# Kernel tuning notes

Measured on AMD Instinct MI355X. Metric: run time of the kernel, lower is better.

## Reference

```python
import jax, jax.numpy as jnp
import numpy as np

N = 100000      # graph nodes
M = 100000      # meta-graph nodes appended after graph nodes
F_IN = 128
HID = 64
NCLASS = 2
E = 1600000
L = 3           # n_layers
ALPHA = 0.2     # LeakyReLU negative slope (args.alpha)


def leaky(x):
    return jax.nn.leaky_relu(x, negative_slope=ALPHA)


def gcn_conv(x, src, dst, W, b, n):
    """PyG GCNConv: add self-loops, symmetric D^-1/2 (A+I) D^-1/2 X W + b."""
    loop = jnp.arange(n, dtype=src.dtype)
    s = jnp.concatenate([src, loop])
    d = jnp.concatenate([dst, loop])
    deg = jax.ops.segment_sum(jnp.ones(d.shape, x.dtype), d, num_segments=n)
    dinv = jnp.where(deg > 0, jax.lax.rsqrt(jnp.maximum(deg, 1.0)), 0.0)
    h = x @ W                                   # [n, out]
    msg = h[s] * (dinv[s] * dinv[d])[:, None]   # gather + edge-normalize
    return jax.ops.segment_sum(msg, d, num_segments=n) + b


def _uniform(k, shape, fan_in):
    s = 1.0 / np.sqrt(fan_in)
    return jax.random.uniform(k, shape, jnp.float32, -s, s)


def setup_inputs():
    key = jax.random.key(0)
    ks = jax.random.split(key, 14)
    x = jax.random.normal(ks[0], (N, F_IN), jnp.float32)
    meta_x = jax.random.normal(ks[1], (M, F_IN), jnp.float32)
    edge_index = jax.random.randint(ks[2], (2, E), 0, N, dtype=jnp.int32)
    # meta_edge_index: node i -> node2idx[i] + N, then add_self_loops over N+M nodes
    node2idx = jax.random.randint(ks[3], (N,), 0, M, dtype=jnp.int32)
    src = jnp.concatenate([jnp.arange(N, dtype=jnp.int32), jnp.arange(N + M, dtype=jnp.int32)])
    dst = jnp.concatenate([node2idx + N, jnp.arange(N + M, dtype=jnp.int32)])
    meta_edge_index = jnp.stack([src, dst])
    params = {
        "W_lin": _uniform(ks[4], (F_IN, HID), F_IN),
        "b_lin": jnp.zeros((HID,), jnp.float32),
        "W_meta_lin": _uniform(ks[5], (F_IN, HID), F_IN),
        "b_meta_lin": jnp.zeros((HID,), jnp.float32),
        "Ws": _uniform(ks[6], (L, HID, HID), HID),
        "bs": jnp.zeros((L, HID), jnp.float32),
        "W_mg": _uniform(ks[7], (HID, HID), HID),
        "b_mg": jnp.zeros((HID,), jnp.float32),
        "W_cls": _uniform(ks[8], (HID, NCLASS), HID),
        "b_cls": jnp.zeros((NCLASS,), jnp.float32),
    }
    return {"x": x, "meta_x": meta_x, "edge_index": edge_index,
            "meta_edge_index": meta_edge_index, **params}


def reference(x, meta_x, edge_index, meta_edge_index,
              W_lin, b_lin, W_meta_lin, b_meta_lin,
              Ws, bs, W_mg, b_mg, W_cls, b_cls):
    h = leaky(x @ W_lin + b_lin)                      # [N, HID]
    mh = leaky(meta_x @ W_meta_lin + b_meta_lin)      # [M, HID]
    src, dst = edge_index[0], edge_index[1]
    for i in range(L):  # dropout is identity in eval mode
        h = leaky(gcn_conv(h, src, dst, Ws[i], bs[i], N))
    z = jnp.concatenate([h, mh], axis=0)              # [N+M, HID]
    z = leaky(gcn_conv(z, meta_edge_index[0], meta_edge_index[1], W_mg, b_mg, N + M))
    logits = z @ W_cls + b_cls                        # [N+M, NCLASS]
    return jax.nn.log_softmax(logits, axis=1)
```

## Files before the change

kernel.cpp:

```cpp
#include <hip/hip_runtime.h>
#include <math.h>

#define ALPHA 0.2f

__device__ __forceinline__ float leaky(float x){ return x > 0.f ? x : ALPHA*x; }
__device__ __forceinline__ float bcast(float v, int l){
  return __int_as_float(__builtin_amdgcn_readlane(__float_as_int(v), l));
}
__device__ __forceinline__ int rdlane_i(int v, int l){
  return __builtin_amdgcn_readlane(v, l);
}

static inline int cdiv(long a, long b){ return (int)((a + b - 1)/b); }

__global__ void k_count_dual(const int* __restrict__ dstA, int nA, int* __restrict__ cntA,
                             const int* __restrict__ dstB, int nB, int* __restrict__ cntB){
  int i = blockIdx.x*blockDim.x + threadIdx.x;
  if(i < nA) atomicAdd(&cntA[dstA[i]], 1);
  else if(i < nA + nB) atomicAdd(&cntB[dstB[i - nA]], 1);
}

__global__ void k_dinv_dual(const int* __restrict__ cntA, float* __restrict__ dinvA, int nA,
                            const int* __restrict__ cntB, float* __restrict__ dinvB, int nB){
  int i = blockIdx.x*blockDim.x + threadIdx.x;
  if(i < nA) dinvA[i] = rsqrtf((float)(cntA[i]+1));
  else if(i < nA + nB){ int j = i - nA; dinvB[j] = rsqrtf((float)(cntB[j]+1)); }
}

__global__ void k_scan1_dual(const int* __restrict__ cntA, int* __restrict__ exA,
                             int* __restrict__ bsA, int nA, int nbA,
                             const int* __restrict__ cntB, int* __restrict__ exB,
                             int* __restrict__ bsB, int nB){
  const int* cnt; int* ex; int* bs; int n; int blk;
  if((int)blockIdx.x < nbA){ cnt=cntA; ex=exA; bs=bsA; n=nA; blk=blockIdx.x; }
  else                     { cnt=cntB; ex=exB; bs=bsB; n=nB; blk=blockIdx.x-nbA; }
  __shared__ int s[256];
  int i = blk*256 + threadIdx.x;
  int v = (i<n) ? cnt[i] : 0;
  s[threadIdx.x]=v; __syncthreads();
  #pragma unroll
  for(int off=1; off<256; off<<=1){
    int t = (threadIdx.x>=(unsigned)off) ? s[threadIdx.x-off] : 0;
    __syncthreads();
    s[threadIdx.x]+=t;
    __syncthreads();
  }
  if(i<n) ex[i] = s[threadIdx.x]-v;
  if(threadIdx.x==255) bs[blk]=s[255];
}

__global__ void k_scan2_dual(int* __restrict__ bsA, int nbA, int* __restrict__ bsB, int nbB){
  __shared__ int s[1024];
  {
    int v = ((int)threadIdx.x<nbA) ? bsA[threadIdx.x] : 0;
    s[threadIdx.x]=v; __syncthreads();
    #pragma unroll
    for(int off=1; off<1024; off<<=1){
      int t = (threadIdx.x>=(unsigned)off) ? s[threadIdx.x-off] : 0;
      __syncthreads();
      s[threadIdx.x]+=t;
      __syncthreads();
    }
    if((int)threadIdx.x<nbA) bsA[threadIdx.x] = s[threadIdx.x]-v;
    __syncthreads();
  }
  {
    int v = ((int)threadIdx.x<nbB) ? bsB[threadIdx.x] : 0;
    s[threadIdx.x]=v; __syncthreads();
    #pragma unroll
    for(int off=1; off<1024; off<<=1){
      int t = (threadIdx.x>=(unsigned)off) ? s[threadIdx.x-off] : 0;
      __syncthreads();
      s[threadIdx.x]+=t;
      __syncthreads();
    }
    if((int)threadIdx.x<nbB) bsB[threadIdx.x] = s[threadIdx.x]-v;
  }
}

__global__ void k_scan3_dual(int* __restrict__ exA, const int* __restrict__ bsA,
                             int nA, int nbA, int totA,
                             int* __restrict__ exB, const int* __restrict__ bsB,
                             int nB, int totB){
  int* ex; const int* bs; int n; int blk; int tot;
  if((int)blockIdx.x < nbA){ ex=exA; bs=bsA; n=nA; blk=blockIdx.x; tot=totA; }
  else                     { ex=exB; bs=bsB; n=nB; blk=blockIdx.x-nbA; tot=totB; }
  int i = blk*256 + threadIdx.x;
  if(i<n && blk>0) ex[i] += bs[blk];
  if(blk==0 && threadIdx.x==0) ex[n] = tot;
}

__global__ void k_fill_dual(const int* __restrict__ eiA, int nA,
                            const int* __restrict__ rpA, int* __restrict__ curA,
                            int* __restrict__ ceA,
                            const int* __restrict__ eiB, int nB,
                            const int* __restrict__ rpB, int* __restrict__ curB,
                            int* __restrict__ ceB){
  int i = blockIdx.x*blockDim.x + threadIdx.x;
  if(i < nA){
    int s = eiA[i], d = eiA[nA + i];
    int pos = rpA[d] + atomicAdd(&curA[d], 1);
    ceA[pos] = s;
  } else if(i < nA + nB){
    int j = i - nA;
    int s = eiB[j], d = eiB[nB + j];
    int pos = rpB[d] + atomicAdd(&curB[d], 1);
    ceB[pos] = s;
  }
}

template<int K, int LEAKY_IN, int EPI>
__global__ __launch_bounds__(256) void k_gemm(const float* __restrict__ X,
                                              const float* __restrict__ W,
                                              const float* __restrict__ b,
                                              float* __restrict__ out, int rows){
  int lane = threadIdx.x & 63;
  int gw = (blockIdx.x*256 + threadIdx.x) >> 6;
  int nw = (gridDim.x*256) >> 6;
  float wcol[K];
  #pragma unroll
  for(int k=0;k<K;k++) wcol[k] = W[(size_t)k*64 + lane];
  float bl = EPI ? b[lane] : 0.f;
  for(int row = gw; row < rows; row += nw){
    const float* xr = X + (size_t)row*K;
    float a0=0.f, a1=0.f, a2=0.f, a3=0.f;
    #pragma unroll
    for(int kk=0; kk<K; kk+=64){
      float xv = xr[kk + lane];
      if(LEAKY_IN) xv = leaky(xv);
      #pragma unroll
      for(int k=0;k<64;k+=4){
        a0 = fmaf(bcast(xv, k+0), wcol[kk+k+0], a0);
        a1 = fmaf(bcast(xv, k+1), wcol[kk+k+1], a1);
        a2 = fmaf(bcast(xv, k+2), wcol[kk+k+2], a2);
        a3 = fmaf(bcast(xv, k+3), wcol[kk+k+3], a3);
      }
    }
    float r = (a0+a1)+(a2+a3);
    if(EPI) r = leaky(r + bl);
    out[(size_t)row*64 + lane] = r;
  }
}

__device__ __forceinline__ float agg_acc(const float* __restrict__ h2,
                                         const int* __restrict__ rowptr,
                                         const int* __restrict__ ce,
                                         const float* __restrict__ dinv,
                                         const float* __restrict__ b,
                                         int i, int c){
  float dv = dinv[i];
  int start = rowptr[i], end = rowptr[i+1];
  float a0 = b[c] + h2[(size_t)i*64+c]*dv*dv, a1=0.f, a2=0.f, a3=0.f;
  int lane8 = c & 7;
  for(int j = start; j < end; j += 8){
    int idx = j + lane8; idx = (idx < end) ? idx : end-1;
    int sv = ce[idx];
    float dwv = dinv[sv];
    #pragma unroll
    for(int k=0;k<8;k+=4){
      int   s0 = rdlane_i(sv, k+0), s1 = rdlane_i(sv, k+1);
      int   s2 = rdlane_i(sv, k+2), s3 = rdlane_i(sv, k+3);
      float w0 = bcast(dwv, k+0), w1 = bcast(dwv, k+1);
      float w2 = bcast(dwv, k+2), w3 = bcast(dwv, k+3);
      float g0 = h2[(size_t)s0*64 + c];
      float g1 = h2[(size_t)s1*64 + c];
      float g2 = h2[(size_t)s2*64 + c];
      float g3 = h2[(size_t)s3*64 + c];
      w0 = (j+k+0 < end) ? w0*dv : 0.f;
      w1 = (j+k+1 < end) ? w1*dv : 0.f;
      w2 = (j+k+2 < end) ? w2*dv : 0.f;
      w3 = (j+k+3 < end) ? w3*dv : 0.f;
      a0 = fmaf(g0, w0, a0);
      a1 = fmaf(g1, w1, a1);
      a2 = fmaf(g2, w2, a2);
      a3 = fmaf(g3, w3, a3);
    }
  }
  return (a0+a1)+(a2+a3);
}

template<int LEAKY_OUT>
__global__ __launch_bounds__(256) void k_aggregate(const float* __restrict__ h2,
                            const int* __restrict__ rowptr,
                            const int* __restrict__ ce,
                            const float* __restrict__ dinv, const float* __restrict__ b,
                            float* __restrict__ out, int n){
  int tid = blockIdx.x*blockDim.x + threadIdx.x;
  int i = tid>>6, c = tid&63;
  if(i>=n) return;
  float acc = agg_acc(h2, rowptr, ce, dinv, b, i, c);
  out[(size_t)i*64+c] = LEAKY_OUT ? leaky(acc) : acc;
}

__global__ __launch_bounds__(256) void k_agg_cls(const float* __restrict__ h2,
                            const int* __restrict__ rowptr,
                            const int* __restrict__ ce,
                            const float* __restrict__ dinv, const float* __restrict__ b,
                            const float* __restrict__ Wc, const float* __restrict__ bc,
                            float* __restrict__ out, int n){
  int tid = blockIdx.x*blockDim.x + threadIdx.x;
  int i = tid>>6, c = tid&63;
  if(i>=n) return;
  float acc = agg_acc(h2, rowptr, ce, dinv, b, i, c);
  float zv = leaky(acc);
  float s0 = zv * Wc[c*2+0];
  float s1 = zv * Wc[c*2+1];
  #pragma unroll
  for(int off=32; off; off>>=1){
    s0 += __shfl_down(s0, off);
    s1 += __shfl_down(s1, off);
  }
  if(c==0){
    float l0 = s0 + bc[0], l1 = s1 + bc[1];
    float m  = fmaxf(l0,l1);
    float lse = m + logf(expf(l0-m)+expf(l1-m));
    out[(size_t)i*2+0] = l0 - lse;
    out[(size_t)i*2+1] = l1 - lse;
  }
}

extern "C" void kernel_launch(void* const* d_in, const int* in_sizes, int n_in,
                              void* d_out, int out_size, void* d_ws, size_t ws_size,
                              hipStream_t stream) {
  const float* x      = (const float*)d_in[0];
  const float* meta_x = (const float*)d_in[1];
  const int*   ei     = (const int*)d_in[2];
  const int*   mei    = (const int*)d_in[3];
  const float* W_lin  = (const float*)d_in[4];
  const float* b_lin  = (const float*)d_in[5];
  const float* W_meta = (const float*)d_in[6];
  const float* b_meta = (const float*)d_in[7];
  const float* Ws     = (const float*)d_in[8];
  const float* bs_    = (const float*)d_in[9];
  const float* W_mg   = (const float*)d_in[10];
  const float* b_mg   = (const float*)d_in[11];
  const float* W_cls  = (const float*)d_in[12];
  const float* b_cls  = (const float*)d_in[13];
  float* out = (float*)d_out;

  const int N  = in_sizes[0]/128;
  const int M  = in_sizes[1]/128;
  const int E  = in_sizes[2]/2;
  const int ME = in_sizes[3]/2;
  const int NM = N + M;

  char* ws = (char*)d_ws;
  size_t off = 0;
  auto alloc = [&](size_t bytes)->void*{ void* p = ws + off; off += (bytes + 255) & ~(size_t)255; return p; };
  float* zbuf  = (float*)alloc((size_t)NM*64*4);
  size_t hwords = (size_t)(2*N > NM ? 2*N : NM)*64;
  float* hreg  = (float*)alloc(hwords*4);
  float* hA = hreg, *hB = hreg + (size_t)N*64;
  float* z2 = hreg;
  int*  ce_g = (int*)alloc((size_t)E*4);
  int*  ce_m = (int*)alloc((size_t)ME*4);
  char* zero_base = ws + off;
  int* cnt_g    = (int*)alloc((size_t)N*4);
  int* cnt_m    = (int*)alloc((size_t)NM*4);
  int* cur_g    = (int*)alloc((size_t)N*4);
  int* cur_m    = (int*)alloc((size_t)NM*4);
  size_t zero_bytes = (ws + off) - zero_base;
  int* rowptr_g = (int*)alloc((size_t)(N+1)*4);
  int* rowptr_m = (int*)alloc((size_t)(NM+1)*4);
  int* bsumA    = (int*)alloc(1024*4);
  int* bsumB    = (int*)alloc(1024*4);
  float* dinv_g = (float*)alloc((size_t)N*4);
  float* dinv_m = (float*)alloc((size_t)NM*4);
  (void)ws_size; (void)n_in; (void)out_size;

  const int B = 256;
  const int nbA = cdiv(N, 256), nbB = cdiv(NM, 256);

  (void)hipMemsetAsync(zero_base, 0, zero_bytes, stream);

  k_count_dual<<<cdiv((long)E+ME,B), B, 0, stream>>>(ei+E, E, cnt_g, mei+ME, ME, cnt_m);
  k_dinv_dual<<<cdiv((long)N+NM,B), B, 0, stream>>>(cnt_g, dinv_g, N, cnt_m, dinv_m, NM);

  k_scan1_dual<<<nbA+nbB, 256, 0, stream>>>(cnt_g, rowptr_g, bsumA, N, nbA,
                                            cnt_m, rowptr_m, bsumB, NM);
  k_scan2_dual<<<1, 1024, 0, stream>>>(bsumA, nbA, bsumB, nbB);
  k_scan3_dual<<<nbA+nbB, 256, 0, stream>>>(rowptr_g, bsumA, N, nbA, E,
                                            rowptr_m, bsumB, NM, ME);
  k_fill_dual<<<cdiv((long)E+ME,B), B, 0, stream>>>(ei, E, rowptr_g, cur_g, ce_g,
                                                    mei, ME, rowptr_m, cur_m, ce_m);

  k_gemm<128,0,1><<<1024, 256, 0, stream>>>(x,      W_lin,  b_lin,  hA,                 N);
  k_gemm<128,0,1><<<1024, 256, 0, stream>>>(meta_x, W_meta, b_meta, zbuf + (size_t)N*64, M);

  float* cin = hA; float* tmp = hB;
  for(int l=0; l<3; ++l){
    const float* Wl = Ws + (size_t)l*64*64;
    const float* bl = bs_ + (size_t)l*64;
    if(l==0) k_gemm<64,0,0><<<2048, 256, 0, stream>>>(cin, Wl, nullptr, tmp, N);
    else     k_gemm<64,1,0><<<2048, 256, 0, stream>>>(cin, Wl, nullptr, tmp, N);
    if(l<2) k_aggregate<0><<<cdiv(N,4), B, 0, stream>>>(tmp, rowptr_g, ce_g, dinv_g, bl, cin, N);
    else    k_aggregate<1><<<cdiv(N,4), B, 0, stream>>>(tmp, rowptr_g, ce_g, dinv_g, bl, zbuf, N);
  }

  k_gemm<64,0,0><<<2048, 256, 0, stream>>>(zbuf, W_mg, nullptr, z2, NM);
  k_agg_cls<<<cdiv(NM,4), B, 0, stream>>>(z2, rowptr_m, ce_m, dinv_m, b_mg,
                                          W_cls, b_cls, out, NM);
}
```

Baseline: 758.7 us.

## Fuse aggregate-then-transform GCN layers and build CSR via two-level bucketing

Result: slower. 961.6 us (+26.7%).

```diff
diff --git a/kernel.cpp b/kernel.cpp
--- a/kernel.cpp
+++ b/kernel.cpp
@@ -79,55 +79,82 @@
 }
 
 __global__ void k_scan3_dual(int* __restrict__ exA, const int* __restrict__ bsA,
-                             int nA, int nbA, int totA,
+                             int nA, int nbA, int totA, int* __restrict__ bcurA,
                              int* __restrict__ exB, const int* __restrict__ bsB,
-                             int nB, int totB){
-  int* ex; const int* bs; int n; int blk; int tot;
-  if((int)blockIdx.x < nbA){ ex=exA; bs=bsA; n=nA; blk=blockIdx.x; tot=totA; }
-  else                     { ex=exB; bs=bsB; n=nB; blk=blockIdx.x-nbA; tot=totB; }
+                             int nB, int totB, int* __restrict__ bcurB){
+  int* ex; const int* bs; int n; int blk; int tot; int* bcur;
+  if((int)blockIdx.x < nbA){ ex=exA; bs=bsA; n=nA; blk=blockIdx.x; tot=totA; bcur=bcurA; }
+  else                     { ex=exB; bs=bsB; n=nB; blk=blockIdx.x-nbA; tot=totB; bcur=bcurB; }
   int i = blk*256 + threadIdx.x;
-  if(i<n && blk>0) ex[i] += bs[blk];
+  if(i<n){
+    int v = ex[i] + (blk>0 ? bs[blk] : 0);
+    ex[i] = v;
+    if((i&63)==0) bcur[i>>6] = v;
+  }
   if(blk==0 && threadIdx.x==0) ex[n] = tot;
 }
 
-__global__ void k_fill_dual(const int* __restrict__ eiA, int nA,
-                            const int* __restrict__ rpA, int* __restrict__ curA,
-                            int* __restrict__ ceA,
-                            const int* __restrict__ eiB, int nB,
-                            const int* __restrict__ rpB, int* __restrict__ curB,
-                            int* __restrict__ ceB){
+__global__ void k_bucket_dual(const int* __restrict__ eiA, int nA,
+                              int* __restrict__ bcurA, int2* __restrict__ tmpA,
+                              const int* __restrict__ eiB, int nB,
+                              int* __restrict__ bcurB, int2* __restrict__ tmpB){
   int i = blockIdx.x*blockDim.x + threadIdx.x;
   if(i < nA){
-    int s = eiA[i], d = eiA[nA + i];
-    int pos = rpA[d] + atomicAdd(&curA[d], 1);
-    ceA[pos] = s;
+    int s = eiA[i], d = eiA[nA+i];
+    int pos = atomicAdd(&bcurA[d>>6], 1);
+    tmpA[pos] = make_int2(s, d);
   } else if(i < nA + nB){
     int j = i - nA;
-    int s = eiB[j], d = eiB[nB + j];
-    int pos = rpB[d] + atomicAdd(&curB[d], 1);
-    ceB[pos] = s;
-  }
-}
-
-template<int K, int LEAKY_IN, int EPI>
-__global__ __launch_bounds__(256) void k_gemm(const float* __restrict__ X,
-                                              const float* __restrict__ W,
-                                              const float* __restrict__ b,
-                                              float* __restrict__ out, int rows){
+    int s = eiB[j], d = eiB[nB+j];
+    int pos = atomicAdd(&bcurB[d>>6], 1);
+    tmpB[pos] = make_int2(s, d);
+  }
+}
+
+__global__ __launch_bounds__(256) void k_place_dual(
+    const int2* __restrict__ tmpA, const int* __restrict__ rpA, int* __restrict__ ceA,
+    int nnA, int nbkA,
+    const int2* __restrict__ tmpB, const int* __restrict__ rpB, int* __restrict__ ceB,
+    int nnB){
+  const int2* tmp; const int* rp; int* ce; int nn; int b;
+  if((int)blockIdx.x < nbkA){ tmp=tmpA; rp=rpA; ce=ceA; nn=nnA; b=blockIdx.x; }
+  else                      { tmp=tmpB; rp=rpB; ce=ceB; nn=nnB; b=blockIdx.x-nbkA; }
+  __shared__ int lcur[64];
+  __shared__ int lrp[65];
+  int base = b<<6;
+  int t = threadIdx.x;
+  if(t<65){
+    int node = base + t; if(node > nn) node = nn;
+    lrp[t] = rp[node];
+    if(t<64) lcur[t] = 0;
+  }
+  __syncthreads();
+  int start = lrp[0], end = lrp[64];
+  for(int j = start + t; j < end; j += 256){
+    int2 r = tmp[j];
+    int dl = r.y - base;
+    int pos = lrp[dl] + atomicAdd(&lcur[dl], 1);
+    ce[pos] = r.x;
+  }
+}
+
+__global__ __launch_bounds__(256) void k_linear128(const float* __restrict__ X,
+                                                   const float* __restrict__ W,
+                                                   const float* __restrict__ b,
+                                                   float* __restrict__ out, int rows){
   int lane = threadIdx.x & 63;
   int gw = (blockIdx.x*256 + threadIdx.x) >> 6;
   int nw = (gridDim.x*256) >> 6;
-  float wcol[K];
+  float wcol[128];
   #pragma unroll
-  for(int k=0;k<K;k++) wcol[k] = W[(size_t)k*64 + lane];
-  float bl = EPI ? b[lane] : 0.f;
+  for(int k=0;k<128;k++) wcol[k] = W[(size_t)k*64 + lane];
+  float bl = b[lane];
   for(int row = gw; row < rows; row += nw){
-    const float* xr = X + (size_t)row*K;
+    const float* xr = X + (size_t)row*128;
     float a0=0.f, a1=0.f, a2=0.f, a3=0.f;
     #pragma unroll
-    for(int kk=0; kk<K; kk+=64){
+    for(int kk=0; kk<128; kk+=64){
       float xv = xr[kk + lane];
-      if(LEAKY_IN) xv = leaky(xv);
       #pragma unroll
       for(int k=0;k<64;k+=4){
         a0 = fmaf(bcast(xv, k+0), wcol[kk+k+0], a0);
@@ -136,86 +163,79 @@
         a3 = fmaf(bcast(xv, k+3), wcol[kk+k+3], a3);
       }
     }
-    float r = (a0+a1)+(a2+a3);
-    if(EPI) r = leaky(r + bl);
-    out[(size_t)row*64 + lane] = r;
-  }
-}
-
-__device__ __forceinline__ float agg_acc(const float* __restrict__ h2,
-                                         const int* __restrict__ rowptr,
-                                         const int* __restrict__ ce,
-                                         const float* __restrict__ dinv,
-                                         const float* __restrict__ b,
-                                         int i, int c){
-  float dv = dinv[i];
-  int start = rowptr[i], end = rowptr[i+1];
-  float a0 = b[c] + h2[(size_t)i*64+c]*dv*dv, a1=0.f, a2=0.f, a3=0.f;
-  int lane8 = c & 7;
-  for(int j = start; j < end; j += 8){
-    int idx = j + lane8; idx = (idx < end) ? idx : end-1;
-    int sv = ce[idx];
-    float dwv = dinv[sv];
+    out[(size_t)row*64 + lane] = leaky(((a0+a1)+(a2+a3)) + bl);
+  }
+}
+
+template<int CLS>
+__global__ __launch_bounds__(256) void k_layer(const float* __restrict__ h,
+                const int* __restrict__ rowptr, const int* __restrict__ ce,
+                const float* __restrict__ dinv,
+                const float* __restrict__ W, const float* __restrict__ b,
+                const float* __restrict__ Wc, const float* __restrict__ bc,
+                float* __restrict__ out, int n){
+  int lane = threadIdx.x & 63;
+  int gw = (blockIdx.x*256 + threadIdx.x) >> 6;
+  int nw = (gridDim.x*256) >> 6;
+  float wcol[64];
+  #pragma unroll
+  for(int k=0;k<64;k++) wcol[k] = W[(size_t)k*64 + lane];
+  float bl = b[lane];
+  float wc0 = CLS ? Wc[lane*2+0] : 0.f;
+  float wc1 = CLS ? Wc[lane*2+1] : 0.f;
+  int lane8 = lane & 7;
+  for(int i = gw; i < n; i += nw){
+    float dv = dinv[i];
+    int start = rowptr[i], end = rowptr[i+1];
+    float a0 = h[(size_t)i*64+lane]*dv*dv, a1=0.f, a2=0.f, a3=0.f;
+    for(int j = start; j < end; j += 8){
+      int idx = j + lane8; idx = (idx < end) ? idx : end-1;
+      int sv = ce[idx];
+      float dwv = dinv[sv];
+      #pragma unroll
+      for(int k=0;k<8;k+=4){
+        int   s0 = rdlane_i(sv,k+0), s1 = rdlane_i(sv,k+1);
+        int   s2 = rdlane_i(sv,k+2), s3 = rdlane_i(sv,k+3);
+        float w0 = bcast(dwv,k+0), w1 = bcast(dwv,k+1);
+        float w2 = bcast(dwv,k+2), w3 = bcast(dwv,k+3);
+        float g0 = h[(size_t)s0*64+lane], g1 = h[(size_t)s1*64+lane];
+        float g2 = h[(size_t)s2*64+lane], g3 = h[(size_t)s3*64+lane];
+        w0 = (j+k+0 < end) ? w0*dv : 0.f;
+        w1 = (j+k+1 < end) ? w1*dv : 0.f;
+        w2 = (j+k+2 < end) ? w2*dv : 0.f;
+        w3 = (j+k+3 < end) ? w3*dv : 0.f;
+        a0 = fmaf(g0,w0,a0); a1 = fmaf(g1,w1,a1);
+        a2 = fmaf(g2,w2,a2); a3 = fmaf(g3,w3,a3);
+      }
+    }
+    float av = (a0+a1)+(a2+a3);
+    float r0=0.f,r1=0.f,r2=0.f,r3=0.f;
     #pragma unroll
-    for(int k=0;k<8;k+=4){
-      int   s0 = rdlane_i(sv, k+0), s1 = rdlane_i(sv, k+1);
-      int   s2 = rdlane_i(sv, k+2), s3 = rdlane_i(sv, k+3);
-      float w0 = bcast(dwv, k+0), w1 = bcast(dwv, k+1);
-      float w2 = bcast(dwv, k+2), w3 = bcast(dwv, k+3);
-      float g0 = h2[(size_t)s0*64 + c];
-      float g1 = h2[(size_t)s1*64 + c];
-      float g2 = h2[(size_t)s2*64 + c];
-      float g3 = h2[(size_t)s3*64 + c];
-      w0 = (j+k+0 < end) ? w0*dv : 0.f;
-      w1 = (j+k+1 < end) ? w1*dv : 0.f;
-      w2 = (j+k+2 < end) ? w2*dv : 0.f;
-      w3 = (j+k+3 < end) ? w3*dv : 0.f;
-      a0 = fmaf(g0, w0, a0);
-      a1 = fmaf(g1, w1, a1);
-      a2 = fmaf(g2, w2, a2);
-      a3 = fmaf(g3, w3, a3);
-    }
-  }
-  return (a0+a1)+(a2+a3);
-}
-
-template<int LEAKY_OUT>
-__global__ __launch_bounds__(256) void k_aggregate(const float* __restrict__ h2,
-                            const int* __restrict__ rowptr,
-                            const int* __restrict__ ce,
-                            const float* __restrict__ dinv, const float* __restrict__ b,
-                            float* __restrict__ out, int n){
-  int tid = blockIdx.x*blockDim.x + threadIdx.x;
-  int i = tid>>6, c = tid&63;
-  if(i>=n) return;
-  float acc = agg_acc(h2, rowptr, ce, dinv, b, i, c);
-  out[(size_t)i*64+c] = LEAKY_OUT ? leaky(acc) : acc;
-}
-
-__global__ __launch_bounds__(256) void k_agg_cls(const float* __restrict__ h2,
-                            const int* __restrict__ rowptr,
-                            const int* __restrict__ ce,
-                            const float* __restrict__ dinv, const float* __restrict__ b,
-                            const float* __restrict__ Wc, const float* __restrict__ bc,
-                            float* __restrict__ out, int n){
-  int tid = blockIdx.x*blockDim.x + threadIdx.x;
-  int i = tid>>6, c = tid&63;
-  if(i>=n) return;
-  float acc = agg_acc(h2, rowptr, ce, dinv, b, i, c);
-  float zv = leaky(acc);
-  float s0 = zv * Wc[c*2+0];
-  float s1 = zv * Wc[c*2+1];
-  #pragma unroll
-  for(int off=32; off; off>>=1){
-    s0 += __shfl_down(s0, off);
-    s1 += __shfl_down(s1, off);
-  }
-  if(c==0){
-    float l0 = s0 + bc[0], l1 = s1 + bc[1];
-    float m  = fmaxf(l0,l1);
-    float lse = m + logf(expf(l0-m)+expf(l1-m));
-    out[(size_t)i*2+0] = l0 - lse;
-    out[(size_t)i*2+1] = l1 - lse;
+    for(int k=0;k<64;k+=4){
+      r0 = fmaf(bcast(av,k+0), wcol[k+0], r0);
+      r1 = fmaf(bcast(av,k+1), wcol[k+1], r1);
+      r2 = fmaf(bcast(av,k+2), wcol[k+2], r2);
+      r3 = fmaf(bcast(av,k+3), wcol[k+3], r3);
+    }
+    float r = ((r0+r1)+(r2+r3)) + bl;
+    if(!CLS){
+      out[(size_t)i*64+lane] = leaky(r);
+    } else {
+      float zv = leaky(r);
+      float s0 = zv*wc0, s1 = zv*wc1;
+      #pragma unroll
+      for(int off2=32; off2; off2>>=1){
+        s0 += __shfl_down(s0, off2);
+        s1 += __shfl_down(s1, off2);
+      }
+      if(lane==0){
+        float l0 = s0 + bc[0], l1 = s1 + bc[1];
+        float m = fmaxf(l0,l1);
+        float lse = m + logf(expf(l0-m)+expf(l1-m));
+        out[(size_t)i*2+0] = l0 - lse;
+        out[(size_t)i*2+1] = l1 - lse;
+      }
+    }
   }
 }
 
@@ -247,23 +267,24 @@
   char* ws = (char*)d_ws;
   size_t off = 0;
   auto alloc = [&](size_t bytes)->void*{ void* p = ws + off; off += (bytes + 255) & ~(size_t)255; return p; };
-  float* zbuf  = (float*)alloc((size_t)NM*64*4);
-  size_t hwords = (size_t)(2*N > NM ? 2*N : NM)*64;
-  float* hreg  = (float*)alloc(hwords*4);
-  float* hA = hreg, *hB = hreg + (size_t)N*64;
-  float* z2 = hreg;
-  int*  ce_g = (int*)alloc((size_t)E*4);
-  int*  ce_m = (int*)alloc((size_t)ME*4);
+  float* zbuf = (float*)alloc((size_t)NM*64*4);
+  float* P0   = (float*)alloc((size_t)N*64*4);
+  float* P1   = (float*)alloc((size_t)N*64*4);
+  int*  ce_g  = (int*)alloc((size_t)E*4);
+  int*  ce_m  = (int*)alloc((size_t)ME*4);
+  int2* tmp_g = (int2*)alloc((size_t)E*8);
+  int2* tmp_m = (int2*)alloc((size_t)ME*8);
   char* zero_base = ws + off;
-  int* cnt_g    = (int*)alloc((size_t)N*4);
-  int* cnt_m    = (int*)alloc((size_t)NM*4);
-  int* cur_g    = (int*)alloc((size_t)N*4);
-  int* cur_m    = (int*)alloc((size_t)NM*4);
+  int* cnt_g  = (int*)alloc((size_t)N*4);
+  int* cnt_m  = (int*)alloc((size_t)NM*4);
   size_t zero_bytes = (ws + off) - zero_base;
   int* rowptr_g = (int*)alloc((size_t)(N+1)*4);
   int* rowptr_m = (int*)alloc((size_t)(NM+1)*4);
-  int* bsumA    = (int*)alloc(1024*4);
-  int* bsumB    = (int*)alloc(1024*4);
+  const int NBg = cdiv(N, 64), NBm = cdiv(NM, 64);
+  int* bcur_g = (int*)alloc((size_t)NBg*4);
+  int* bcur_m = (int*)alloc((size_t)NBm*4);
+  int* bsumA  = (int*)alloc(1024*4);
+  int* bsumB  = (int*)alloc(1024*4);
   float* dinv_g = (float*)alloc((size_t)N*4);
   float* dinv_m = (float*)alloc((size_t)NM*4);
   (void)ws_size; (void)n_in; (void)out_size;
@@ -279,25 +300,24 @@
   k_scan1_dual<<<nbA+nbB, 256, 0, stream>>>(cnt_g, rowptr_g, bsumA, N, nbA,
                                             cnt_m, rowptr_m, bsumB, NM);
   k_scan2_dual<<<1, 1024, 0, stream>>>(bsumA, nbA, bsumB, nbB);
-  k_scan3_dual<<<nbA+nbB, 256, 0, stream>>>(rowptr_g, bsumA, N, nbA, E,
-                                            rowptr_m, bsumB, NM, ME);
-  k_fill_dual<<<cdiv((long)E+ME,B), B, 0, stream>>>(ei, E, rowptr_g, cur_g, ce_g,
-                                                    mei, ME, rowptr_m, cur_m, ce_m);
-
-  k_gemm<128,0,1><<<1024, 256, 0, stream>>>(x,      W_lin,  b_lin,  hA,                 N);
-  k_gemm<128,0,1><<<1024, 256, 0, stream>>>(meta_x, W_meta, b_meta, zbuf + (size_t)N*64, M);
-
-  float* cin = hA; float* tmp = hB;
-  for(int l=0; l<3; ++l){
-    const float* Wl = Ws + (size_t)l*64*64;
-    const float* bl = bs_ + (size_t)l*64;
-    if(l==0) k_gemm<64,0,0><<<2048, 256, 0, stream>>>(cin, Wl, nullptr, tmp, N);
-    else     k_gemm<64,1,0><<<2048, 256, 0, stream>>>(cin, Wl, nullptr, tmp, N);
-    if(l<2) k_aggregate<0><<<cdiv(N,4), B, 0, stream>>>(tmp, rowptr_g, ce_g, dinv_g, bl, cin, N);
-    else    k_aggregate<1><<<cdiv(N,4), B, 0, stream>>>(tmp, rowptr_g, ce_g, dinv_g, bl, zbuf, N);
-  }
-
-  k_gemm<64,0,0><<<2048, 256, 0, stream>>>(zbuf, W_mg, nullptr, z2, NM);
-  k_agg_cls<<<cdiv(NM,4), B, 0, stream>>>(z2, rowptr_m, ce_m, dinv_m, b_mg,
-                                          W_cls, b_cls, out, NM);
-}
+  k_scan3_dual<<<nbA+nbB, 256, 0, stream>>>(rowptr_g, bsumA, N, nbA, E, bcur_g,
+                                            rowptr_m, bsumB, NM, ME, bcur_m);
+
+  k_bucket_dual<<<cdiv((long)E+ME,B), B, 0, stream>>>(ei, E, bcur_g, tmp_g,
+                                                      mei, ME, bcur_m, tmp_m);
+  k_place_dual<<<NBg+NBm, 256, 0, stream>>>(tmp_g, rowptr_g, ce_g, N, NBg,
+                                            tmp_m, rowptr_m, ce_m, NM);
+
+  k_linear128<<<1024, 256, 0, stream>>>(x,      W_lin,  b_lin,  P0,                  N);
+  k_linear128<<<1024, 256, 0, stream>>>(meta_x, W_meta, b_meta, zbuf + (size_t)N*64, M);
+
+  k_layer<0><<<1024, 256, 0, stream>>>(P0, rowptr_g, ce_g, dinv_g,
+                                       Ws,              bs_,      nullptr, nullptr, P1,   N);
+  k_layer<0><<<1024, 256, 0, stream>>>(P1, rowptr_g, ce_g, dinv_g,
+                                       Ws + 64*64,      bs_ + 64, nullptr, nullptr, P0,   N);
+  k_layer<0><<<1024, 256, 0, stream>>>(P0, rowptr_g, ce_g, dinv_g,
+                                       Ws + 2*64*64,    bs_ +128, nullptr, nullptr, zbuf, N);
+
+  k_layer<1><<<1024, 256, 0, stream>>>(zbuf, rowptr_m, ce_m, dinv_m,
+                                       W_mg, b_mg, W_cls, b_cls, out, NM);
+}
```
